# Kernel tuning notes

Hardware: AMD Instinct MI355X
Metric: run time of the kernel (lower is better)

## Reference

```python
import jax, jax.numpy as jnp
import numpy as np

N_NODES = 100000
DEG = 16
N_EDGES = N_NODES * DEG
D_IN = 64
D_OUT = 64


def setup_inputs() -> dict:
    key = jax.random.key(0)
    k1, k2, k3 = jax.random.split(key, 3)
    X = jax.random.normal(k1, (N_NODES, D_IN), dtype=jnp.float32)
    stdv = 1.0 / np.sqrt(D_OUT)
    weight = jax.random.uniform(k2, (D_IN, D_OUT), dtype=jnp.float32, minval=-stdv, maxval=stdv)
    # CSR: fixed out-degree DEG per node (regularized for reproducible setup)
    row_pointers = (jnp.arange(N_NODES + 1, dtype=jnp.int64) * DEG)
    column_index = jax.random.randint(k3, (N_EDGES,), 0, N_NODES, dtype=jnp.int32)
    # GCN normalization: degrees[i] = 1/sqrt(d_i)
    counts = (row_pointers[1:] - row_pointers[:-1]).astype(jnp.float32)
    degrees = 1.0 / jnp.sqrt(jnp.maximum(counts, 1.0))
    return {"X": X, "weight": weight, "row_pointers": row_pointers,
            "column_index": column_index, "degrees": degrees}


def reference(X, weight, row_pointers, column_index, degrees):
    # Feature transform first (D_OUT <= D_IN keeps aggregation traffic low)
    xw = X @ weight                                   # [N, D_OUT]
    counts = row_pointers[1:] - row_pointers[:-1]     # [N]
    dst = jnp.repeat(jnp.arange(N_NODES, dtype=jnp.int32), counts,
                     total_repeat_length=N_EDGES)     # [E] destination node per edge
    src = column_index                                # [E] neighbor (source) per edge
    norm = degrees[dst] * degrees[src]                # [E] d_i^{-1/2} d_j^{-1/2}
    msgs = xw[src] * norm[:, None]                    # [E, D_OUT]
    out = jax.ops.segment_sum(msgs, dst, num_segments=N_NODES)  # [N, D_OUT]
    return out
```

## Files before the change

### kernel.cpp

```cpp
#include <hip/hip_runtime.h>

#define D 64

__global__ __launch_bounds__(256, 4)
void gcn_fused_kernel(const float* __restrict__ X,
                      const float* __restrict__ W,
                      const int* __restrict__ rp,
                      const int* __restrict__ col,
                      const float* __restrict__ deg,
                      float* __restrict__ out,
                      int n_nodes)
{
    const int lane = threadIdx.x & 63;
    const int gwave = (int)((blockIdx.x * blockDim.x + threadIdx.x) >> 6);
    const int nwaves = (int)((gridDim.x * blockDim.x) >> 6);

    float wcol[D];
#pragma unroll
    for (int l = 0; l < D; ++l) wcol[l] = W[l * D + lane];

    for (int node = gwave; node < n_nodes; node += nwaves) {
        const int start = rp[node];
        const int end   = rp[node + 1];
        const float di  = deg[node];

        float h0 = 0.f, h1 = 0.f, h2 = 0.f, h3 = 0.f;
        const int cnt_total = end - start;

        if (cnt_total == 16) {
            int   s_  = (lane < 16) ? col[start + lane] : 0;
            float nm_ = (lane < 16) ? di * deg[s_] : 0.f;
#pragma unroll
            for (int j = 0; j < 16; j += 4) {
                const int s0 = __builtin_amdgcn_readlane(s_, j + 0);
                const int s1 = __builtin_amdgcn_readlane(s_, j + 1);
                const int s2 = __builtin_amdgcn_readlane(s_, j + 2);
                const int s3 = __builtin_amdgcn_readlane(s_, j + 3);
                const float n0 = __uint_as_float(__builtin_amdgcn_readlane(__float_as_uint(nm_), j + 0));
                const float n1 = __uint_as_float(__builtin_amdgcn_readlane(__float_as_uint(nm_), j + 1));
                const float n2 = __uint_as_float(__builtin_amdgcn_readlane(__float_as_uint(nm_), j + 2));
                const float n3 = __uint_as_float(__builtin_amdgcn_readlane(__float_as_uint(nm_), j + 3));
                h0 = fmaf(n0, X[s0 * D + lane], h0);
                h1 = fmaf(n1, X[s1 * D + lane], h1);
                h2 = fmaf(n2, X[s2 * D + lane], h2);
                h3 = fmaf(n3, X[s3 * D + lane], h3);
            }
        } else {
            for (int e0 = start; e0 < end; e0 += 64) {
                const int cnt = min(64, end - e0);
                int   s_  = (lane < cnt) ? col[e0 + lane] : 0;
                float nm_ = (lane < cnt) ? di * deg[s_] : 0.f;
                for (int j = 0; j < cnt; ++j) {
                    const int   sj = __builtin_amdgcn_readlane(s_, j);
                    const float nj = __uint_as_float(__builtin_amdgcn_readlane(__float_as_uint(nm_), j));
                    h0 = fmaf(nj, X[sj * D + lane], h0);
                }
            }
        }
        const float h = (h0 + h1) + (h2 + h3);

        float a0 = 0.f, a1 = 0.f, a2 = 0.f, a3 = 0.f;
#pragma unroll
        for (int l = 0; l < D; l += 4) {
            const float b0 = __uint_as_float(__builtin_amdgcn_readlane(__float_as_uint(h), l + 0));
            const float b1 = __uint_as_float(__builtin_amdgcn_readlane(__float_as_uint(h), l + 1));
            const float b2 = __uint_as_float(__builtin_amdgcn_readlane(__float_as_uint(h), l + 2));
            const float b3 = __uint_as_float(__builtin_amdgcn_readlane(__float_as_uint(h), l + 3));
            a0 = fmaf(b0, wcol[l + 0], a0);
            a1 = fmaf(b1, wcol[l + 1], a1);
            a2 = fmaf(b2, wcol[l + 2], a2);
            a3 = fmaf(b3, wcol[l + 3], a3);
        }
        out[(size_t)node * D + lane] = (a0 + a1) + (a2 + a3);
    }
}

extern "C" void kernel_launch(void* const* d_in, const int* in_sizes, int n_in,
                              void* d_out, int out_size, void* d_ws, size_t ws_size,
                              hipStream_t stream) {
    const float* X   = (const float*)d_in[0];
    const float* W   = (const float*)d_in[1];
    const int*   rp  = (const int*)d_in[2];
    const int*   col = (const int*)d_in[3];
    const float* deg = (const float*)d_in[4];
    float* out = (float*)d_out;

    const int n_nodes = in_sizes[4];

    const int blocks = 1024;
    gcn_fused_kernel<<<blocks, 256, 0, stream>>>(X, W, rp, col, deg, out, n_nodes);
}
```

Measured before the change: 139.6 us.

## Split into XW transform to bf16 workspace and a paired-node gather kernel

```diff
diff --git a/kernel.cpp b/kernel.cpp
--- a/kernel.cpp
+++ b/kernel.cpp
@@ -1,18 +1,19 @@
 #include <hip/hip_runtime.h>
+#include <hip/hip_bf16.h>
 
 #define D 64
 
-__global__ __launch_bounds__(256, 4)
-void gcn_fused_kernel(const float* __restrict__ X,
-                      const float* __restrict__ W,
-                      const int* __restrict__ rp,
-                      const int* __restrict__ col,
-                      const float* __restrict__ deg,
-                      float* __restrict__ out,
-                      int n_nodes)
+static __device__ __forceinline__ float bcast_f(float v, int l) {
+    return __uint_as_float(__builtin_amdgcn_readlane(__float_as_uint(v), l));
+}
+
+__global__ __launch_bounds__(256, 2)
+void xw_scale_kernel(const float* __restrict__ X, const float* __restrict__ W,
+                     const float* __restrict__ deg, ushort* __restrict__ Y,
+                     int n_nodes)
 {
-    const int lane = threadIdx.x & 63;
-    const int gwave = (int)((blockIdx.x * blockDim.x + threadIdx.x) >> 6);
+    const int lane   = threadIdx.x & 63;
+    const int gwave  = (int)((blockIdx.x * blockDim.x + threadIdx.x) >> 6);
     const int nwaves = (int)((gridDim.x * blockDim.x) >> 6);
 
     float wcol[D];
@@ -20,58 +21,118 @@
     for (int l = 0; l < D; ++l) wcol[l] = W[l * D + lane];
 
     for (int node = gwave; node < n_nodes; node += nwaves) {
+        const float xr = X[(size_t)node * D + lane];
+        const float dn = deg[node];
+        float a0 = 0.f, a1 = 0.f, a2 = 0.f, a3 = 0.f;
+#pragma unroll
+        for (int l = 0; l < D; l += 4) {
+            a0 = fmaf(bcast_f(xr, l + 0), wcol[l + 0], a0);
+            a1 = fmaf(bcast_f(xr, l + 1), wcol[l + 1], a1);
+            a2 = fmaf(bcast_f(xr, l + 2), wcol[l + 2], a2);
+            a3 = fmaf(bcast_f(xr, l + 3), wcol[l + 3], a3);
+        }
+        const float r = ((a0 + a1) + (a2 + a3)) * dn;
+        const uint32_t u = __float_as_uint(r);
+        Y[(size_t)node * D + lane] = (ushort)((u + 0x7fffu + ((u >> 16) & 1u)) >> 16);
+    }
+}
+
+__global__ __launch_bounds__(256, 4)
+void gather_kernel(const ushort* __restrict__ Y, const int* __restrict__ rp,
+                   const int* __restrict__ col, const float* __restrict__ deg,
+                   float* __restrict__ out, int n_nodes)
+{
+    const int lane   = threadIdx.x & 63;
+    const int gwave  = (int)((blockIdx.x * blockDim.x + threadIdx.x) >> 6);
+    const int nwaves = (int)((gridDim.x * blockDim.x) >> 6);
+    const int npairs = (n_nodes + 1) >> 1;
+
+    for (int p = gwave; p < npairs; p += nwaves) {
+        const int nA = 2 * p, nB = 2 * p + 1;
+        const bool hasB = (nB < n_nodes);
+        const int a0 = rp[nA], a1 = rp[nA + 1];
+        const int b0 = hasB ? rp[nB] : 0;
+        const int b1 = hasB ? rp[nB + 1] : 0;
+
+        if ((a1 - a0) == 16 && (!hasB || (b1 - b0) == 16)) {
+            int s_ = 0;
+            if (lane < 16)        s_ = col[a0 + lane];
+            else if (lane < 32)   s_ = hasB ? col[b0 + (lane & 15)] : 0;
+
+            const int half  = lane >> 5;
+            const int feat2 = lane & 31;
+
+            float accx = 0.f, accy = 0.f;
+#pragma unroll
+            for (int j = 0; j < 16; ++j) {
+                const int sa = __builtin_amdgcn_readlane(s_, j);
+                const int sb = __builtin_amdgcn_readlane(s_, 16 + j);
+                const int s  = half ? sb : sa;
+                const uint32_t u =
+                    *(const uint32_t*)(Y + (size_t)s * D + feat2 * 2);
+                accx += __uint_as_float(u << 16);
+                accy += __uint_as_float(u & 0xffff0000u);
+            }
+            const int nd = half ? nB : nA;
+            const float dn = (half && !hasB) ? 0.f : deg[nd];
+            if (!half || hasB) {
+                float2 v; v.x = accx * dn; v.y = accy * dn;
+                *(float2*)(out + (size_t)nd * D + feat2 * 2) = v;
+            }
+        } else {
+            for (int t = 0; t < 2; ++t) {
+                const int nd = t ? nB : nA;
+                if (nd >= n_nodes) break;
+                const int st = rp[nd], en = rp[nd + 1];
+                float acc = 0.f;
+                for (int e = st; e < en; ++e) {
+                    const int s = col[e];
+                    const uint32_t w = Y[(size_t)s * D + lane];
+                    acc += __uint_as_float(w << 16);
+                }
+                out[(size_t)nd * D + lane] = acc * deg[nd];
+            }
+        }
+    }
+}
+
+__global__ __launch_bounds__(256, 4)
+void gcn_fused_kernel(const float* __restrict__ X, const float* __restrict__ W,
+                      const int* __restrict__ rp, const int* __restrict__ col,
+                      const float* __restrict__ deg, float* __restrict__ out,
+                      int n_nodes)
+{
+    const int lane   = threadIdx.x & 63;
+    const int gwave  = (int)((blockIdx.x * blockDim.x + threadIdx.x) >> 6);
+    const int nwaves = (int)((gridDim.x * blockDim.x) >> 6);
+
+    for (int node = gwave; node < n_nodes; node += nwaves) {
         const int start = rp[node];
         const int end   = rp[node + 1];
         const float di  = deg[node];
+        float h0 = 0.f, h1 = 0.f, h2 = 0.f, h3 = 0.f;
 
-        float h0 = 0.f, h1 = 0.f, h2 = 0.f, h3 = 0.f;
-        const int cnt_total = end - start;
-
-        if (cnt_total == 16) {
-            int   s_  = (lane < 16) ? col[start + lane] : 0;
-            float nm_ = (lane < 16) ? di * deg[s_] : 0.f;
-#pragma unroll
-            for (int j = 0; j < 16; j += 4) {
-                const int s0 = __builtin_amdgcn_readlane(s_, j + 0);
-                const int s1 = __builtin_amdgcn_readlane(s_, j + 1);
-                const int s2 = __builtin_amdgcn_readlane(s_, j + 2);
-                const int s3 = __builtin_amdgcn_readlane(s_, j + 3);
-                const float n0 = __uint_as_float(__builtin_amdgcn_readlane(__float_as_uint(nm_), j + 0));
-                const float n1 = __uint_as_float(__builtin_amdgcn_readlane(__float_as_uint(nm_), j + 1));
-                const float n2 = __uint_as_float(__builtin_amdgcn_readlane(__float_as_uint(nm_), j + 2));
-                const float n3 = __uint_as_float(__builtin_amdgcn_readlane(__float_as_uint(nm_), j + 3));
-                h0 = fmaf(n0, X[s0 * D + lane], h0);
-                h1 = fmaf(n1, X[s1 * D + lane], h1);
-                h2 = fmaf(n2, X[s2 * D + lane], h2);
-                h3 = fmaf(n3, X[s3 * D + lane], h3);
-            }
-        } else {
-            for (int e0 = start; e0 < end; e0 += 64) {
-                const int cnt = min(64, end - e0);
-                int   s_  = (lane < cnt) ? col[e0 + lane] : 0;
-                float nm_ = (lane < cnt) ? di * deg[s_] : 0.f;
-                for (int j = 0; j < cnt; ++j) {
-                    const int   sj = __builtin_amdgcn_readlane(s_, j);
-                    const float nj = __uint_as_float(__builtin_amdgcn_readlane(__float_as_uint(nm_), j));
-                    h0 = fmaf(nj, X[sj * D + lane], h0);
-                }
+        for (int e0 = start; e0 < end; e0 += 64) {
+            const int cnt = min(64, end - e0);
+            int   s_  = (lane < cnt) ? col[e0 + lane] : 0;
+            float nm_ = (lane < cnt) ? di * deg[s_] : 0.f;
+            for (int j = 0; j < cnt; ++j) {
+                const int   sj = __builtin_amdgcn_readlane(s_, j);
+                const float nj = bcast_f(nm_, j);
+                h0 = fmaf(nj, X[(size_t)sj * D + lane], h0);
             }
         }
         const float h = (h0 + h1) + (h2 + h3);
 
-        float a0 = 0.f, a1 = 0.f, a2 = 0.f, a3 = 0.f;
+        float c0 = 0.f, c1 = 0.f, c2 = 0.f, c3 = 0.f;
 #pragma unroll
         for (int l = 0; l < D; l += 4) {
-            const float b0 = __uint_as_float(__builtin_amdgcn_readlane(__float_as_uint(h), l + 0));
-            const float b1 = __uint_as_float(__builtin_amdgcn_readlane(__float_as_uint(h), l + 1));
-            const float b2 = __uint_as_float(__builtin_amdgcn_readlane(__float_as_uint(h), l + 2));
-            const float b3 = __uint_as_float(__builtin_amdgcn_readlane(__float_as_uint(h), l + 3));
-            a0 = fmaf(b0, wcol[l + 0], a0);
-            a1 = fmaf(b1, wcol[l + 1], a1);
-            a2 = fmaf(b2, wcol[l + 2], a2);
-            a3 = fmaf(b3, wcol[l + 3], a3);
+            c0 = fmaf(bcast_f(h, l + 0), W[(l + 0) * D + lane], c0);
+            c1 = fmaf(bcast_f(h, l + 1), W[(l + 1) * D + lane], c1);
+            c2 = fmaf(bcast_f(h, l + 2), W[(l + 2) * D + lane], c2);
+            c3 = fmaf(bcast_f(h, l + 3), W[(l + 3) * D + lane], c3);
         }
-        out[(size_t)node * D + lane] = (a0 + a1) + (a2 + a3);
+        out[(size_t)node * D + lane] = (c0 + c1) + (c2 + c3);
     }
 }
 
@@ -86,7 +147,13 @@
     float* out = (float*)d_out;
 
     const int n_nodes = in_sizes[4];
+    const size_t y_bytes = (size_t)n_nodes * D * sizeof(ushort);
 
-    const int blocks = 1024;
-    gcn_fused_kernel<<<blocks, 256, 0, stream>>>(X, W, rp, col, deg, out, n_nodes);
+    if (ws_size >= y_bytes) {
+        ushort* Y = (ushort*)d_ws;
+        xw_scale_kernel<<<1024, 256, 0, stream>>>(X, W, deg, Y, n_nodes);
+        gather_kernel<<<2048, 256, 0, stream>>>(Y, rp, col, deg, out, n_nodes);
+    } else {
+        gcn_fused_kernel<<<1024, 256, 0, stream>>>(X, W, rp, col, deg, out, n_nodes);
+    }
 }
```

Measured after the change: 132.8 us. 1.05x faster.
